# Performance work log

Measured on AMD Instinct MI355X. Metric: run time of the kernel, lower is better.

Reference implementation:

```python
import jax, jax.numpy as jnp
import numpy as np

B, K, S, L, D, A = 16, 128, 64, 2, 256, 500  # batch, beam, stack, layers, hidden, max_actions


def setup_inputs() -> dict:
    key = jax.random.key(0)
    k = jax.random.split(key, 8)
    return {
        "gen_ll": jax.random.normal(k[0], (B, K), jnp.float32),
        "trees": jax.random.normal(k[1], (B, K, S, D), jnp.float32),
        "hiddens": jax.random.normal(k[2], (B, K, S + 1, L, D), jnp.float32),
        "cells": jax.random.normal(k[3], (B, K, S + 1, L, D), jnp.float32),
        "actions": jax.random.randint(k[4], (B, K, A), 0, 100, dtype=jnp.int64)
        if jax.config.jax_enable_x64 else jax.random.randint(k[4], (B, K, A), 0, 100),
        "actions_pos": jax.random.randint(k[5], (B, K), 0, A - 1),
        "pointer": jax.random.randint(k[6], (B, K), 0, S),
        "beam_widths": jax.random.randint(k[7], (B,), 1, K + 1),  # >= 1 active beam per batch
    }


def _gather_beam(x, sort_idx):
    # gather along beam dim (axis=1) with broadcast over trailing dims
    idx = sort_idx.reshape(sort_idx.shape + (1,) * (x.ndim - 2))
    return jnp.take_along_axis(x, idx, axis=1)


def reference(gen_ll, trees, hiddens, cells, actions, actions_pos, pointer, beam_widths):
    # BeamItems.shrink(): mask beams outside active width, sort by score desc,
    # then reorder every parallel tensor (stack + action path) by sort_idx.
    order = jnp.arange(K)
    active = order[None, :] < beam_widths[:, None]                    # [B, K] active_idx_mask
    gen_ll_m = jnp.where(active, gen_ll, -jnp.inf)
    sort_idx = jnp.argsort(-gen_ll_m, axis=1)                          # descending sort
    gen_ll_s = jnp.take_along_axis(gen_ll_m, sort_idx, axis=1)

    trees_s = _gather_beam(trees, sort_idx)                            # stack.sort_by
    hiddens_s = _gather_beam(hiddens, sort_idx)
    cells_s = _gather_beam(cells, sort_idx)
    actions_s = _gather_beam(actions, sort_idx)                        # action_path.sort_by
    actions_pos_s = jnp.take_along_axis(actions_pos, sort_idx, axis=1)
    pointer_s = jnp.take_along_axis(pointer, sort_idx, axis=1)         # stack_state.sort_by

    new_beam_widths = jnp.minimum(beam_widths, K)
    # BeamItems.marginal_probs(): logsumexp over active beams (inactive already -inf)
    marginal = jax.nn.logsumexp(gen_ll_s, axis=1)                      # [B]
    # ActionPath.prev_actions(): gather at actions_pos
    prev_actions = jnp.take_along_axis(actions_s, actions_pos_s[:, :, None], axis=2)[:, :, 0]

    return (gen_ll_s, trees_s, hiddens_s, cells_s, marginal,
            actions_s, actions_pos_s, pointer_s, prev_actions, new_beam_widths)
```

## Files before the change

### kernel.cpp

```cpp
#include <hip/hip_runtime.h>
#include <math.h>

#define B 16
#define K 128
#define S 64
#define L 2
#define D 256
#define A 500

#define ROW4_TREES 4096
#define HALF4_HID  4160

#define NEG_BIG (-1.0e30f)

typedef float f32x4 __attribute__((ext_vector_type(4)));
typedef int   i32x4 __attribute__((ext_vector_type(4)));

#define OFF_GENLL 0
#define OFF_TREES 2048
#define OFF_HID   33556480
#define OFF_CELLS 101713920
#define OFF_MARG  169871360
#define OFF_ACT   169871376
#define OFF_APOS  170895376
#define OFF_PTR   170897424
#define OFF_PREV  170899472
#define OFF_NBW   170901520

#define NBLK 2048
#define NU_TREES 2048
#define UPB 5

template<int N4>
__device__ __forceinline__ void copy_unit(const f32x4* __restrict__ s,
                                          f32x4* __restrict__ d, int tid)
{
    constexpr int FULL = N4 / 256;
    constexpr int REM  = N4 % 256;
    for (int g = 0; g < FULL; g += 8) {
        f32x4 v[8];
#pragma unroll
        for (int i = 0; i < 8; ++i)
            v[i] = __builtin_nontemporal_load(&s[(g + i) * 256 + tid]);
#pragma unroll
        for (int i = 0; i < 8; ++i)
            __builtin_nontemporal_store(v[i], &d[(g + i) * 256 + tid]);
    }
    if (REM && tid < REM) {
        f32x4 v = __builtin_nontemporal_load(&s[FULL * 256 + tid]);
        __builtin_nontemporal_store(v, &d[FULL * 256 + tid]);
    }
}

__global__ void __launch_bounds__(256, 8)
k_fused(const float* __restrict__ gen_ll,
        const f32x4* __restrict__ trees,
        const f32x4* __restrict__ hiddens,
        const f32x4* __restrict__ cells,
        const int* __restrict__ actions,
        const int* __restrict__ actions_pos,
        const int* __restrict__ pointer,
        const int* __restrict__ beam_widths,
        float* __restrict__ out)
{
    __shared__ float key[B][K];
    __shared__ int   sidx[B][K];
    __shared__ int   wbuf[B];
    __shared__ float red[4];

    const int tid = threadIdx.x;
    const int bid = blockIdx.x;

    if (tid < B) wbuf[tid] = beam_widths[tid];
    __syncthreads();
    for (int t = tid; t < B * K; t += 256) {
        const int b = t >> 7, i = t & 127;
        key[b][i] = (i < wbuf[b]) ? gen_ll[t] : NEG_BIG;
    }
    __syncthreads();
    for (int t = tid; t < B * K; t += 256) {
        const int b = t >> 7, i = t & 127;
        const float my = key[b][i];
        int rank = 0;
#pragma unroll 16
        for (int ii = 0; ii < K; ++ii) {
            const float ki = key[b][ii];
            rank += (ki > my) || (ki == my && ii < i);
        }
        sidx[b][rank] = i;
    }
    __syncthreads();

    const int u0 = bid * UPB;
#pragma unroll
    for (int q = 0; q < UPB; ++q) {
        const int u = u0 + q;
        if (u < NU_TREES) {
            const int b = u >> 7, k = u & 127;
            const int j = sidx[b][k];
            copy_unit<ROW4_TREES>(trees + (size_t)(b * K + j) * ROW4_TREES,
                                  (f32x4*)(out + OFF_TREES) + (size_t)u * ROW4_TREES,
                                  tid);
        } else {
            const int u2 = u - NU_TREES;
            const int which = u2 >> 12;
            const int u3 = u2 & 4095;
            const int row = u3 >> 1, half = u3 & 1;
            const int b = row >> 7, k = row & 127;
            const int j = sidx[b][k];
            const f32x4* src = (which ? cells : hiddens)
                             + ((size_t)(b * K + j) * 2 + half) * HALF4_HID;
            f32x4* dst = (f32x4*)(out + (which ? OFF_CELLS : OFF_HID))
                       + (size_t)u3 * HALF4_HID;
            copy_unit<HALF4_HID>(src, dst, tid);
        }
    }

    {
        const int b = bid >> 7, k = bid & 127;
        const int j = sidx[b][k];
        const i32x4* s = (const i32x4*)actions + (size_t)(b * K + j) * 125;
        f32x4* d = (f32x4*)(out + OFF_ACT) + (size_t)bid * 125;
        if (tid < 125) {
            const i32x4 v = __builtin_nontemporal_load(&s[tid]);
            f32x4 f;
            f.x = (float)v.x; f.y = (float)v.y; f.z = (float)v.z; f.w = (float)v.w;
            __builtin_nontemporal_store(f, &d[tid]);
        }
    }

    if (bid < B) {
        const int b = bid;
        if (tid < K) {
            const int j = sidx[b][tid];
            out[OFF_GENLL + b * K + tid] = key[b][j];
            const int ap = actions_pos[b * K + j];
            out[OFF_APOS + b * K + tid] = (float)ap;
            out[OFF_PTR  + b * K + tid] = (float)pointer[b * K + j];
            out[OFF_PREV + b * K + tid] = (float)actions[(size_t)(b * K + j) * A + ap];
        }
        const float v = (tid < K) ? key[b][tid] : NEG_BIG;
        if (tid < 128) {
            float m = v;
#pragma unroll
            for (int mask = 32; mask >= 1; mask >>= 1)
                m = fmaxf(m, __shfl_xor(m, mask, 64));
            if ((tid & 63) == 0) red[tid >> 6] = m;
        }
        __syncthreads();
        const float m = fmaxf(red[0], red[1]);
        if (tid < 128) {
            float e = expf(v - m);
#pragma unroll
            for (int mask = 32; mask >= 1; mask >>= 1)
                e += __shfl_xor(e, mask, 64);
            if ((tid & 63) == 0) red[2 + (tid >> 6)] = e;
        }
        __syncthreads();
        if (tid == 0) {
            out[OFF_MARG + b] = m + logf(red[2] + red[3]);
            const int w = wbuf[b];
            out[OFF_NBW + b] = (float)(w < K ? w : K);
        }
    }
}

extern "C" void kernel_launch(void* const* d_in, const int* in_sizes, int n_in,
                              void* d_out, int out_size, void* d_ws, size_t ws_size,
                              hipStream_t stream)
{
    const float* gen_ll      = (const float*)d_in[0];
    const float* trees       = (const float*)d_in[1];
    const float* hiddens     = (const float*)d_in[2];
    const float* cells       = (const float*)d_in[3];
    const int*   actions     = (const int*)d_in[4];
    const int*   actions_pos = (const int*)d_in[5];
    const int*   pointer     = (const int*)d_in[6];
    const int*   beam_widths = (const int*)d_in[7];
    float* out = (float*)d_out;

    k_fused<<<NBLK, 256, 0, stream>>>(gen_ll, (const f32x4*)trees,
                                      (const f32x4*)hiddens, (const f32x4*)cells,
                                      actions, actions_pos, pointer, beam_widths, out);
}
```

Measured before the change: 288.2 us.

## Split sort into separate small kernel and pass sort indices via workspace

Previously each of the 2048 copy blocks redundantly recomputed the full rank-sort for all 16 batches in shared memory before copying. Now a 16-block kernel computes the sort indices once, writes the small outputs and marginals, and stores the indices in workspace. The copy kernel then reads them from global memory. This removes redundant per-block sort work and shared-memory use, at the cost of a second launch and a serial dependency between the two kernels.

```diff
diff --git a/kernel.cpp b/kernel.cpp
--- a/kernel.cpp
+++ b/kernel.cpp
@@ -52,44 +52,74 @@
     }
 }
 
-__global__ void __launch_bounds__(256, 8)
-k_fused(const float* __restrict__ gen_ll,
-        const f32x4* __restrict__ trees,
-        const f32x4* __restrict__ hiddens,
-        const f32x4* __restrict__ cells,
-        const int* __restrict__ actions,
-        const int* __restrict__ actions_pos,
-        const int* __restrict__ pointer,
-        const int* __restrict__ beam_widths,
-        float* __restrict__ out)
+__global__ void __launch_bounds__(128)
+k_sort(const float* __restrict__ gen_ll,
+       const int* __restrict__ actions,
+       const int* __restrict__ actions_pos,
+       const int* __restrict__ pointer,
+       const int* __restrict__ beam_widths,
+       float* __restrict__ out,
+       int* __restrict__ sort_idx)
 {
-    __shared__ float key[B][K];
-    __shared__ int   sidx[B][K];
-    __shared__ int   wbuf[B];
+    const int b = blockIdx.x;
+    const int k = threadIdx.x;
+
+    __shared__ float key[K];
+    __shared__ int   sidx[K];
     __shared__ float red[4];
 
+    const int w = beam_widths[b];
+    const float my = (k < w) ? gen_ll[b * K + k] : NEG_BIG;
+    key[k] = my;
+    __syncthreads();
+
+    int rank = 0;
+#pragma unroll 16
+    for (int i = 0; i < K; ++i) {
+        const float ki = key[i];
+        rank += (ki > my) || (ki == my && i < k);
+    }
+    sidx[rank] = k;
+    __syncthreads();
+
+    const int j = sidx[k];
+    sort_idx[b * K + k] = j;
+
+    out[OFF_GENLL + b * K + k] = key[j];
+    const int ap = actions_pos[b * K + j];
+    out[OFF_APOS + b * K + k] = (float)ap;
+    out[OFF_PTR  + b * K + k] = (float)pointer[b * K + j];
+    out[OFF_PREV + b * K + k] = (float)actions[(size_t)(b * K + j) * A + ap];
+
+    float m = my;
+#pragma unroll
+    for (int mask = 32; mask >= 1; mask >>= 1)
+        m = fmaxf(m, __shfl_xor(m, mask, 64));
+    if ((k & 63) == 0) red[k >> 6] = m;
+    __syncthreads();
+    m = fmaxf(red[0], red[1]);
+    float e = expf(my - m);
+#pragma unroll
+    for (int mask = 32; mask >= 1; mask >>= 1)
+        e += __shfl_xor(e, mask, 64);
+    if ((k & 63) == 0) red[2 + (k >> 6)] = e;
+    __syncthreads();
+    if (k == 0) {
+        out[OFF_MARG + b] = m + logf(red[2] + red[3]);
+        out[OFF_NBW + b] = (float)(w < K ? w : K);
+    }
+}
+
+__global__ void __launch_bounds__(256, 8)
+k_copy(const f32x4* __restrict__ trees,
+       const f32x4* __restrict__ hiddens,
+       const f32x4* __restrict__ cells,
+       const int* __restrict__ actions,
+       const int* __restrict__ sort_idx,
+       float* __restrict__ out)
+{
     const int tid = threadIdx.x;
     const int bid = blockIdx.x;
-
-    if (tid < B) wbuf[tid] = beam_widths[tid];
-    __syncthreads();
-    for (int t = tid; t < B * K; t += 256) {
-        const int b = t >> 7, i = t & 127;
-        key[b][i] = (i < wbuf[b]) ? gen_ll[t] : NEG_BIG;
-    }
-    __syncthreads();
-    for (int t = tid; t < B * K; t += 256) {
-        const int b = t >> 7, i = t & 127;
-        const float my = key[b][i];
-        int rank = 0;
-#pragma unroll 16
-        for (int ii = 0; ii < K; ++ii) {
-            const float ki = key[b][ii];
-            rank += (ki > my) || (ki == my && ii < i);
-        }
-        sidx[b][rank] = i;
-    }
-    __syncthreads();
 
     const int u0 = bid * UPB;
 #pragma unroll
@@ -97,7 +127,7 @@
         const int u = u0 + q;
         if (u < NU_TREES) {
             const int b = u >> 7, k = u & 127;
-            const int j = sidx[b][k];
+            const int j = sort_idx[(b << 7) + k];
             copy_unit<ROW4_TREES>(trees + (size_t)(b * K + j) * ROW4_TREES,
                                   (f32x4*)(out + OFF_TREES) + (size_t)u * ROW4_TREES,
                                   tid);
@@ -107,7 +137,7 @@
             const int u3 = u2 & 4095;
             const int row = u3 >> 1, half = u3 & 1;
             const int b = row >> 7, k = row & 127;
-            const int j = sidx[b][k];
+            const int j = sort_idx[(b << 7) + k];
             const f32x4* src = (which ? cells : hiddens)
                              + ((size_t)(b * K + j) * 2 + half) * HALF4_HID;
             f32x4* dst = (f32x4*)(out + (which ? OFF_CELLS : OFF_HID))
@@ -117,8 +147,8 @@
     }
 
     {
-        const int b = bid >> 7, k = bid & 127;
-        const int j = sidx[b][k];
+        const int b = bid >> 7;
+        const int j = sort_idx[bid];
         const i32x4* s = (const i32x4*)actions + (size_t)(b * K + j) * 125;
         f32x4* d = (f32x4*)(out + OFF_ACT) + (size_t)bid * 125;
         if (tid < 125) {
@@ -126,41 +156,6 @@
             f32x4 f;
             f.x = (float)v.x; f.y = (float)v.y; f.z = (float)v.z; f.w = (float)v.w;
             __builtin_nontemporal_store(f, &d[tid]);
-        }
-    }
-
-    if (bid < B) {
-        const int b = bid;
-        if (tid < K) {
-            const int j = sidx[b][tid];
-            out[OFF_GENLL + b * K + tid] = key[b][j];
-            const int ap = actions_pos[b * K + j];
-            out[OFF_APOS + b * K + tid] = (float)ap;
-            out[OFF_PTR  + b * K + tid] = (float)pointer[b * K + j];
-            out[OFF_PREV + b * K + tid] = (float)actions[(size_t)(b * K + j) * A + ap];
-        }
-        const float v = (tid < K) ? key[b][tid] : NEG_BIG;
-        if (tid < 128) {
-            float m = v;
-#pragma unroll
-            for (int mask = 32; mask >= 1; mask >>= 1)
-                m = fmaxf(m, __shfl_xor(m, mask, 64));
-            if ((tid & 63) == 0) red[tid >> 6] = m;
-        }
-        __syncthreads();
-        const float m = fmaxf(red[0], red[1]);
-        if (tid < 128) {
-            float e = expf(v - m);
-#pragma unroll
-            for (int mask = 32; mask >= 1; mask >>= 1)
-                e += __shfl_xor(e, mask, 64);
-            if ((tid & 63) == 0) red[2 + (tid >> 6)] = e;
-        }
-        __syncthreads();
-        if (tid == 0) {
-            out[OFF_MARG + b] = m + logf(red[2] + red[3]);
-            const int w = wbuf[b];
-            out[OFF_NBW + b] = (float)(w < K ? w : K);
         }
     }
 }
@@ -178,8 +173,10 @@
     const int*   pointer     = (const int*)d_in[6];
     const int*   beam_widths = (const int*)d_in[7];
     float* out = (float*)d_out;
+    int* sort_idx = (int*)d_ws;
 
-    k_fused<<<NBLK, 256, 0, stream>>>(gen_ll, (const f32x4*)trees,
-                                      (const f32x4*)hiddens, (const f32x4*)cells,
-                                      actions, actions_pos, pointer, beam_widths, out);
+    k_sort<<<B, K, 0, stream>>>(gen_ll, actions, actions_pos, pointer,
+                                beam_widths, out, sort_idx);
+    k_copy<<<NBLK, 256, 0, stream>>>((const f32x4*)trees, (const f32x4*)hiddens,
+                                     (const f32x4*)cells, actions, sort_idx, out);
 }
```

Result: faster. 272.3 us (-5.5%).
